# Performance work log

Hardware: AMD Instinct MI355X
Metric: run time of the kernel (lower is better)

The kernel has to match this reference:

```python
import jax, jax.numpy as jnp
import numpy as np

N_HEAD = 16
N_EMBD = 1024
TIME_EMBD = 64
EPS = 1e-5

def _ln(x, w, b):
    mu = jnp.mean(x, axis=-1, keepdims=True)
    var = jnp.mean(jnp.square(x - mu), axis=-1, keepdims=True)
    return (x - mu) * jax.lax.rsqrt(var + EPS) * w + b

def _gelu(x):
    return jax.nn.gelu(x, approximate=False)

def setup_inputs() -> dict:
    key = jax.random.key(0)
    ks = jax.random.split(key, 12)
    B, T, D, TE = 2, 2048, N_EMBD, TIME_EMBD
    C = D + TE  # 1088
    s = lambda fan_in: 1.0 / np.sqrt(fan_in)
    return {
        "z": jax.random.normal(ks[0], (B, T, D), jnp.float32),
        "t": jax.random.uniform(ks[1], (B,), jnp.float32),
        # time_mlp: Linear(1, TE) -> GELU -> Linear(TE, TE)
        "w_t1": jax.random.normal(ks[2], (1, TE), jnp.float32) * s(1),
        "b_t1": jnp.zeros((TE,), jnp.float32),
        "w_t2": jax.random.normal(ks[3], (TE, TE), jnp.float32) * s(TE),
        "b_t2": jnp.zeros((TE,), jnp.float32),
        # attention
        "ln_a_w": jnp.ones((C,), jnp.float32),
        "ln_a_b": jnp.zeros((C,), jnp.float32),
        "w_attn": jax.random.normal(ks[4], (C, 3 * D), jnp.float32) * s(C),
        "b_attn": jnp.zeros((3 * D,), jnp.float32),
        "w_proj": jax.random.normal(ks[5], (D, D), jnp.float32) * s(D),
        "b_proj": jnp.zeros((D,), jnp.float32),
        # mlp
        "ln_m_w": jnp.ones((C,), jnp.float32),
        "ln_m_b": jnp.zeros((C,), jnp.float32),
        "w_fc": jax.random.normal(ks[6], (C, 4 * D), jnp.float32) * s(C),
        "b_fc": jnp.zeros((4 * D,), jnp.float32),
        "w_fc2": jax.random.normal(ks[7], (4 * D, D), jnp.float32) * s(4 * D),
        "b_fc2": jnp.zeros((D,), jnp.float32),
    }

def reference(z, t, w_t1, b_t1, w_t2, b_t2, ln_a_w, ln_a_b, w_attn, b_attn,
              w_proj, b_proj, ln_m_w, ln_m_b, w_fc, b_fc, w_fc2, b_fc2):
    B, T, D = z.shape
    H, hd = N_HEAD, N_EMBD // N_HEAD
    # time embedding: [B, TE] broadcast over T
    t_emb = _gelu(t[:, None] @ w_t1 + b_t1) @ w_t2 + b_t2
    t_emb_bt = jnp.broadcast_to(t_emb[:, None, :], (B, T, TIME_EMBD))
    # --- attention with time-conditioned input ---
    zt = jnp.concatenate([z, t_emb_bt], axis=-1)            # [B,T,D+TE]
    x = _ln(zt, ln_a_w, ln_a_b)
    qkv = x @ w_attn + b_attn                               # [B,T,3D]
    q, k, v = jnp.split(qkv, 3, axis=-1)
    q = q.reshape(B, T, H, hd)
    k = k.reshape(B, T, H, hd)
    v = v.reshape(B, T, H, hd)
    att = jnp.einsum('bqhd,bkhd->bhqk', q, k) * (1.0 / np.sqrt(hd))
    mask = jnp.tril(jnp.ones((T, T), bool))
    att = jnp.where(mask, att, -jnp.inf)
    att = jax.nn.softmax(att, axis=-1)
    y = jnp.einsum('bhqk,bkhd->bqhd', att, v).reshape(B, T, D)
    h = y @ w_proj + b_proj                                 # [B,T,D]
    # --- mlp with time-conditioned input ---
    ht = jnp.concatenate([h, t_emb_bt], axis=-1)
    m = _ln(ht, ln_m_w, ln_m_b)
    dz = _gelu(m @ w_fc + b_fc) @ w_fc2 + b_fc2             # [B,T,D]
    return dz
```

## Files before the change

### kernel.cpp

```cpp
#include <hip/hip_runtime.h>
#include <stdint.h>
#include <math.h>

#define T_SEQ 2048
#define NHEAD 16
#define HD 64
#define DMODEL 1024
#define CDIM 1088
#define MROWS 4096

typedef uint16_t u16;
typedef __bf16 b8v __attribute__((ext_vector_type(8)));
typedef float f4v __attribute__((ext_vector_type(4)));

typedef __attribute__((address_space(3))) void lds_void;
typedef const __attribute__((address_space(1))) void glb_void;

__device__ __forceinline__ float b2f(u16 u) {
  union { uint32_t i; float f; } c; c.i = ((uint32_t)u) << 16; return c.f;
}
__device__ __forceinline__ u16 f2b(float f) {
  union { float f; uint32_t i; } c; c.f = f;
  uint32_t x = c.i;
  return (u16)((x + 0x7fffu + ((x >> 16) & 1u)) >> 16);
}
__device__ __forceinline__ float gelu_f(float x) {
  return 0.5f * x * (1.0f + erff(x * 0.70710678118654752f));
}

__global__ void time_mlp_kernel(const float* __restrict__ t, const float* __restrict__ w1,
                                const float* __restrict__ b1, const float* __restrict__ w2,
                                const float* __restrict__ b2, float* __restrict__ temb) {
  __shared__ float h1[2][64];
  int tid = threadIdx.x;
  int b = tid >> 6, i = tid & 63;
  float tv = t[b];
  h1[b][i] = gelu_f(tv * w1[i] + b1[i]);
  __syncthreads();
  float acc = b2[i];
  for (int k = 0; k < 64; ++k) acc += h1[b][k] * w2[k * 64 + i];
  temb[b * 64 + i] = acc;
}

__global__ __launch_bounds__(256) void transpose_kernel(const float* __restrict__ src,
                                                        u16* __restrict__ dst,
                                                        int R, int C) {
  __shared__ u16 tile[32][33];
  int tx = threadIdx.x & 31, ty = threadIdx.x >> 5;
  int c0 = blockIdx.x * 32, r0 = blockIdx.y * 32;
#pragma unroll
  for (int i = 0; i < 4; ++i) {
    int r = ty + i * 8;
    tile[r][tx] = f2b(src[(size_t)(r0 + r) * C + c0 + tx]);
  }
  __syncthreads();
#pragma unroll
  for (int i = 0; i < 4; ++i) {
    int c = ty + i * 8;
    dst[(size_t)(c0 + c) * R + r0 + tx] = tile[tx][c];
  }
}

__global__ __launch_bounds__(256) void ln_concat_kernel(const float* __restrict__ zf,
                                                        const u16* __restrict__ zb,
                                                        const float* __restrict__ temb,
                                                        const float* __restrict__ w,
                                                        const float* __restrict__ bvec,
                                                        u16* __restrict__ xout,
                                                        int in_f32) {
  __shared__ float red[4];
  int row = blockIdx.x;
  int b = row / T_SEQ;
  int tid = threadIdx.x;
  float v[5];
  float sum = 0.f;
#pragma unroll
  for (int i = 0; i < 5; ++i) {
    int c = tid + i * 256;
    float val = 0.f;
    if (c < CDIM) {
      if (c < DMODEL)
        val = in_f32 ? zf[(size_t)row * DMODEL + c] : b2f(zb[(size_t)row * DMODEL + c]);
      else
        val = temb[b * 64 + (c - DMODEL)];
    }
    v[i] = val;
    sum += val;
  }
#pragma unroll
  for (int off = 32; off; off >>= 1) sum += __shfl_xor(sum, off, 64);
  int wv = tid >> 6, ln = tid & 63;
  if (ln == 0) red[wv] = sum;
  __syncthreads();
  float mean = (red[0] + red[1] + red[2] + red[3]) * (1.0f / CDIM);
  __syncthreads();
  float sq = 0.f;
#pragma unroll
  for (int i = 0; i < 5; ++i) {
    int c = tid + i * 256;
    if (c < CDIM) { float d = v[i] - mean; sq += d * d; }
  }
#pragma unroll
  for (int off = 32; off; off >>= 1) sq += __shfl_xor(sq, off, 64);
  if (ln == 0) red[wv] = sq;
  __syncthreads();
  float inv = rsqrtf((red[0] + red[1] + red[2] + red[3]) * (1.0f / CDIM) + 1e-5f);
#pragma unroll
  for (int i = 0; i < 5; ++i) {
    int c = tid + i * 256;
    if (c < CDIM)
      xout[(size_t)row * CDIM + c] = f2b((v[i] - mean) * inv * w[c] + bvec[c]);
  }
}

__global__ __launch_bounds__(256) void gemm_bt_kernel(const u16* __restrict__ A,
                                                      const u16* __restrict__ Bt,
                                                      const float* __restrict__ bias,
                                                      void* __restrict__ Cout,
                                                      int M, int N, int K,
                                                      int do_gelu, int out_f32) {
  __shared__ u16 As[2][128 * 32];
  __shared__ u16 Bs[2][128 * 32];
  const int tid = threadIdx.x;
  const int wave = tid >> 6, lane = tid & 63;
  const int wr = wave >> 1, wc = wave & 1;
  const int m0 = blockIdx.x * 128;
  const int n0 = blockIdx.y * 128;
  const int lrow = lane & 15, quad = lane >> 4;
  const int srow = lane >> 2, sseg = lane & 3;

  const u16* gA0 = A  + (size_t)(m0 + wave * 32 + srow) * K + sseg * 8;
  const u16* gA1 = gA0 + (size_t)16 * K;
  const u16* gB0 = Bt + (size_t)(n0 + wave * 32 + srow) * K + sseg * 8;
  const u16* gB1 = gB0 + (size_t)16 * K;
  const int la0 = (wave * 32) * 32, la1 = (wave * 32 + 16) * 32;

  f4v acc[4][4] = {};

  __builtin_amdgcn_global_load_lds((glb_void*)gA0, (lds_void*)&As[0][la0], 16, 0, 0);
  __builtin_amdgcn_global_load_lds((glb_void*)gA1, (lds_void*)&As[0][la1], 16, 0, 0);
  __builtin_amdgcn_global_load_lds((glb_void*)gB0, (lds_void*)&Bs[0][la0], 16, 0, 0);
  __builtin_amdgcn_global_load_lds((glb_void*)gB1, (lds_void*)&Bs[0][la1], 16, 0, 0);

  int cur = 0;
  for (int k0 = 0; k0 < K; k0 += 32) {
    __syncthreads();
    if (k0 + 32 < K) {
      int nxt = cur ^ 1;
      __builtin_amdgcn_global_load_lds((glb_void*)(gA0 + k0 + 32), (lds_void*)&As[nxt][la0], 16, 0, 0);
      __builtin_amdgcn_global_load_lds((glb_void*)(gA1 + k0 + 32), (lds_void*)&As[nxt][la1], 16, 0, 0);
      __builtin_amdgcn_global_load_lds((glb_void*)(gB0 + k0 + 32), (lds_void*)&Bs[nxt][la0], 16, 0, 0);
      __builtin_amdgcn_global_load_lds((glb_void*)(gB1 + k0 + 32), (lds_void*)&Bs[nxt][la1], 16, 0, 0);
    }
    b8v af[4], bfr[4];
#pragma unroll
    for (int mi = 0; mi < 4; ++mi)
      af[mi] = *(const b8v*)(&As[cur][(wr * 64 + mi * 16 + lrow) * 32 + quad * 8]);
#pragma unroll
    for (int ni = 0; ni < 4; ++ni)
      bfr[ni] = *(const b8v*)(&Bs[cur][(wc * 64 + ni * 16 + lrow) * 32 + quad * 8]);
#pragma unroll
    for (int mi = 0; mi < 4; ++mi)
#pragma unroll
      for (int ni = 0; ni < 4; ++ni)
        acc[mi][ni] = __builtin_amdgcn_mfma_f32_16x16x32_bf16(af[mi], bfr[ni], acc[mi][ni], 0, 0, 0);
    cur ^= 1;
  }

#pragma unroll
  for (int mi = 0; mi < 4; ++mi) {
#pragma unroll
    for (int ni = 0; ni < 4; ++ni) {
      int gcol = n0 + wc * 64 + ni * 16 + lrow;
      float bv = bias[gcol];
#pragma unroll
      for (int r = 0; r < 4; ++r) {
        int grow = m0 + wr * 64 + mi * 16 + quad * 4 + r;
        float v = acc[mi][ni][r] + bv;
        if (do_gelu) v = gelu_f(v);
        if (out_f32)
          ((float*)Cout)[(size_t)grow * N + gcol] = v;
        else
          ((u16*)Cout)[(size_t)grow * N + gcol] = f2b(v);
      }
    }
  }
}

__global__ __launch_bounds__(256) void attn_mfma_kernel(const u16* __restrict__ qkv,
                                                        u16* __restrict__ y) {
  __shared__ u16 Ks[64 * 72];
  __shared__ u16 Vts[64 * 72];
  __shared__ u16 Ps[64 * 72];
  const int bh = blockIdx.x;
  const int b = bh >> 4, h = bh & 15;
  const int qt = 31 - blockIdx.y;
  const int tid = threadIdx.x, w = tid >> 6, lane = tid & 63;
  const int lrow = lane & 15, quad = lane >> 4;
  const int q0 = qt * 64;
  const int qg = q0 + w * 16 + lrow;

  b8v qf[2];
#pragma unroll
  for (int dc = 0; dc < 2; ++dc)
    qf[dc] = *(const b8v*)(qkv + (size_t)(b * T_SEQ + qg) * 3072 + h * 64 + dc * 32 + quad * 8);

  f4v oacc[4] = {};
  float mrun = -__builtin_inff(), lrun = 0.f;

  const int nch = qt + 1;
  for (int ct = 0; ct < nch; ++ct) {
    __syncthreads();
    {
      int r = tid >> 2, sg = tid & 3;
      const u16* src = qkv + (size_t)(b * T_SEQ + ct * 64 + r) * 3072 + h * 64 + 1024 + sg * 16;
      *(uint4*)(&Ks[r * 72 + sg * 16]) = *(const uint4*)(src);
      *(uint4*)(&Ks[r * 72 + sg * 16 + 8]) = *(const uint4*)(src + 8);
    }
    {
      int pr = tid >> 3, dsg = tid & 7;
      const u16* v0 = qkv + (size_t)(b * T_SEQ + ct * 64 + 2 * pr) * 3072 + h * 64 + 2048 + dsg * 8;
      uint4 a = *(const uint4*)(v0);
      uint4 bb = *(const uint4*)(v0 + 3072);
      uint32_t aw[4] = {a.x, a.y, a.z, a.w};
      uint32_t bw[4] = {bb.x, bb.y, bb.z, bb.w};
#pragma unroll
      for (int j = 0; j < 8; ++j) {
        int d = dsg * 8 + j;
        u16 ae = (u16)(aw[j >> 1] >> ((j & 1) * 16));
        u16 be = (u16)(bw[j >> 1] >> ((j & 1) * 16));
        int keyp = (2 * pr) ^ (((d >> 3) & 7) * 8);
        *(uint32_t*)(&Vts[d * 72 + keyp]) = (uint32_t)ae | ((uint32_t)be << 16);
      }
    }
    __syncthreads();

    f4v sacc[4] = {};
#pragma unroll
    for (int ks = 0; ks < 4; ++ks)
#pragma unroll
      for (int dc = 0; dc < 2; ++dc) {
        b8v kf = *(const b8v*)(&Ks[(ks * 16 + lrow) * 72 + dc * 32 + quad * 8]);
        sacc[ks] = __builtin_amdgcn_mfma_f32_16x16x32_bf16(kf, qf[dc], sacc[ks], 0, 0, 0);
      }

    bool diag = (ct == qt);
#pragma unroll
    for (int ks = 0; ks < 4; ++ks)
#pragma unroll
      for (int r = 0; r < 4; ++r) {
        float v = sacc[ks][r] * 0.125f;
        int key = ct * 64 + ks * 16 + quad * 4 + r;
        if (diag && key > qg) v = -__builtin_inff();
        sacc[ks][r] = v;
      }

    float rmax = sacc[0][0];
#pragma unroll
    for (int ks = 0; ks < 4; ++ks)
#pragma unroll
      for (int r = 0; r < 4; ++r) rmax = fmaxf(rmax, sacc[ks][r]);
    rmax = fmaxf(rmax, __shfl_xor(rmax, 16, 64));
    rmax = fmaxf(rmax, __shfl_xor(rmax, 32, 64));
    float mn = fmaxf(mrun, rmax);
    float al = __expf(mrun - mn);
    mrun = mn;
    float psum = 0.f;
#pragma unroll
    for (int ks = 0; ks < 4; ++ks)
#pragma unroll
      for (int r = 0; r < 4; ++r) {
        float p = __expf(sacc[ks][r] - mn);
        sacc[ks][r] = p;
        psum += p;
      }
    psum += __shfl_xor(psum, 16, 64);
    psum += __shfl_xor(psum, 32, 64);
    lrun = lrun * al + psum;
#pragma unroll
    for (int ds = 0; ds < 4; ++ds) oacc[ds] *= al;

#pragma unroll
    for (int ks = 0; ks < 4; ++ks) {
      ushort4 pw;
      pw.x = f2b(sacc[ks][0]); pw.y = f2b(sacc[ks][1]);
      pw.z = f2b(sacc[ks][2]); pw.w = f2b(sacc[ks][3]);
      *(ushort4*)(&Ps[(w * 16 + lrow) * 72 + ks * 16 + quad * 4]) = pw;
    }

    b8v pf[2];
#pragma unroll
    for (int kc = 0; kc < 2; ++kc)
      pf[kc] = *(const b8v*)(&Ps[(w * 16 + lrow) * 72 + kc * 32 + quad * 8]);
#pragma unroll
    for (int ds = 0; ds < 4; ++ds)
#pragma unroll
      for (int kc = 0; kc < 2; ++kc) {
        int d = ds * 16 + lrow;
        int off = (kc * 32 + quad * 8) ^ (((d >> 3) & 7) * 8);
        b8v vfv = *(const b8v*)(&Vts[d * 72 + off]);
        oacc[ds] = __builtin_amdgcn_mfma_f32_16x16x32_bf16(vfv, pf[kc], oacc[ds], 0, 0, 0);
      }
  }

  float rinv = 1.0f / lrun;
  u16* yrow = y + (size_t)(b * T_SEQ + qg) * DMODEL + h * 64;
#pragma unroll
  for (int ds = 0; ds < 4; ++ds) {
    ushort4 ov;
    ov.x = f2b(oacc[ds][0] * rinv);
    ov.y = f2b(oacc[ds][1] * rinv);
    ov.z = f2b(oacc[ds][2] * rinv);
    ov.w = f2b(oacc[ds][3] * rinv);
    *(ushort4*)(yrow + ds * 16 + quad * 4) = ov;
  }
}

extern "C" void kernel_launch(void* const* d_in, const int* in_sizes, int n_in,
                              void* d_out, int out_size, void* d_ws, size_t ws_size,
                              hipStream_t stream) {
  const float* z      = (const float*)d_in[0];
  const float* t      = (const float*)d_in[1];
  const float* w_t1   = (const float*)d_in[2];
  const float* b_t1   = (const float*)d_in[3];
  const float* w_t2   = (const float*)d_in[4];
  const float* b_t2   = (const float*)d_in[5];
  const float* ln_a_w = (const float*)d_in[6];
  const float* ln_a_b = (const float*)d_in[7];
  const float* w_attn = (const float*)d_in[8];
  const float* b_attn = (const float*)d_in[9];
  const float* w_proj = (const float*)d_in[10];
  const float* b_proj = (const float*)d_in[11];
  const float* ln_m_w = (const float*)d_in[12];
  const float* ln_m_b = (const float*)d_in[13];
  const float* w_fc   = (const float*)d_in[14];
  const float* b_fc   = (const float*)d_in[15];
  const float* w_fc2  = (const float*)d_in[16];
  const float* b_fc2  = (const float*)d_in[17];

  char* ws = (char*)d_ws;
  float* temb  = (float*)ws;
  u16* wT_attn = (u16*)(ws + 1024);
  u16* wT_proj = wT_attn + (size_t)3072 * 1088;
  u16* wT_fc   = wT_proj + (size_t)1024 * 1024;
  u16* wT_fc2  = wT_fc   + (size_t)4096 * 1088;
  u16* xbuf    = wT_fc2  + (size_t)1024 * 4096;
  u16* big     = xbuf    + (size_t)4096 * 1088;
  u16* ybuf    = big     + (size_t)4096 * 4096;
  u16* hbuf    = ybuf    + (size_t)4096 * 1024;

  time_mlp_kernel<<<dim3(1), dim3(128), 0, stream>>>(t, w_t1, b_t1, w_t2, b_t2, temb);

  transpose_kernel<<<dim3(3072 / 32, 1088 / 32), dim3(256), 0, stream>>>(w_attn, wT_attn, 1088, 3072);
  transpose_kernel<<<dim3(1024 / 32, 1024 / 32), dim3(256), 0, stream>>>(w_proj, wT_proj, 1024, 1024);
  transpose_kernel<<<dim3(4096 / 32, 1088 / 32), dim3(256), 0, stream>>>(w_fc, wT_fc, 1088, 4096);
  transpose_kernel<<<dim3(1024 / 32, 4096 / 32), dim3(256), 0, stream>>>(w_fc2, wT_fc2, 4096, 1024);

  ln_concat_kernel<<<dim3(MROWS), dim3(256), 0, stream>>>(z, (const u16*)nullptr, temb,
                                                          ln_a_w, ln_a_b, xbuf, 1);

  gemm_bt_kernel<<<dim3(MROWS / 128, 3072 / 128), dim3(256), 0, stream>>>(
      xbuf, wT_attn, b_attn, big, MROWS, 3072, 1088, 0, 0);

  attn_mfma_kernel<<<dim3(32, 32), dim3(256), 0, stream>>>(big, ybuf);

  gemm_bt_kernel<<<dim3(MROWS / 128, 1024 / 128), dim3(256), 0, stream>>>(
      ybuf, wT_proj, b_proj, hbuf, MROWS, 1024, 1024, 0, 0);

  ln_concat_kernel<<<dim3(MROWS), dim3(256), 0, stream>>>((const float*)nullptr, hbuf, temb,
                                                          ln_m_w, ln_m_b, xbuf, 0);

  gemm_bt_kernel<<<dim3(MROWS / 128, 4096 / 128), dim3(256), 0, stream>>>(
      xbuf, wT_fc, b_fc, big, MROWS, 4096, 1088, 1, 0);

  gemm_bt_kernel<<<dim3(MROWS / 128, 1024 / 128), dim3(256), 0, stream>>>(
      big, wT_fc2, b_fc2, d_out, MROWS, 1024, 4096, 0, 1);
}
```

Measured before the change: 426.8 us.

## Split-K the proj and fc2 GEMMs in two and reduce the partial sums

The two N=1024 GEMMs (attention projection and fc2) launched only 256 blocks, which underfills the GPU's CUs. A new split-K=2 GEMM writes fp32 partial results to two buffers, giving 512 blocks. The projection partials are summed inside the LN kernel through a new mode, and the fc2 partials are summed by a small add kernel. In exchange this adds fp32 partial-buffer write and read traffic, plus one extra launch for the final add.

```diff
diff --git a/kernel.cpp b/kernel.cpp
--- a/kernel.cpp
+++ b/kernel.cpp
@@ -61,13 +61,24 @@
   }
 }
 
+__global__ __launch_bounds__(256) void add2_kernel(const float4* __restrict__ a,
+                                                   const float4* __restrict__ b,
+                                                   float4* __restrict__ o, int n4) {
+  int i = blockIdx.x * 256 + threadIdx.x;
+  if (i < n4) {
+    float4 x = a[i], y = b[i];
+    o[i] = float4{x.x + y.x, x.y + y.y, x.z + y.z, x.w + y.w};
+  }
+}
+
 __global__ __launch_bounds__(256) void ln_concat_kernel(const float* __restrict__ zf,
+                                                        const float* __restrict__ zf2,
                                                         const u16* __restrict__ zb,
                                                         const float* __restrict__ temb,
                                                         const float* __restrict__ w,
                                                         const float* __restrict__ bvec,
                                                         u16* __restrict__ xout,
-                                                        int in_f32) {
+                                                        int mode) {
   __shared__ float red[4];
   int row = blockIdx.x;
   int b = row / T_SEQ;
@@ -79,10 +90,14 @@
     int c = tid + i * 256;
     float val = 0.f;
     if (c < CDIM) {
-      if (c < DMODEL)
-        val = in_f32 ? zf[(size_t)row * DMODEL + c] : b2f(zb[(size_t)row * DMODEL + c]);
-      else
+      if (c < DMODEL) {
+        size_t idx = (size_t)row * DMODEL + c;
+        if (mode == 0) val = b2f(zb[idx]);
+        else if (mode == 1) val = zf[idx];
+        else val = zf[idx] + zf2[idx];
+      } else {
         val = temb[b * 64 + (c - DMODEL)];
+      }
     }
     v[i] = val;
     sum += val;
@@ -182,6 +197,77 @@
           ((float*)Cout)[(size_t)grow * N + gcol] = v;
         else
           ((u16*)Cout)[(size_t)grow * N + gcol] = f2b(v);
+      }
+    }
+  }
+}
+
+__global__ __launch_bounds__(256) void gemm_splitk2_kernel(const u16* __restrict__ A,
+                                                           const u16* __restrict__ Bt,
+                                                           const float* __restrict__ bias,
+                                                           float* __restrict__ C0,
+                                                           float* __restrict__ C1,
+                                                           int M, int N, int K, int Kc) {
+  __shared__ u16 As[2][128 * 32];
+  __shared__ u16 Bs[2][128 * 32];
+  const int tid = threadIdx.x;
+  const int wave = tid >> 6, lane = tid & 63;
+  const int wr = wave >> 1, wc = wave & 1;
+  const int m0 = blockIdx.x * 128;
+  const int n0 = blockIdx.y * 128;
+  const int kz = blockIdx.z;
+  const int lrow = lane & 15, quad = lane >> 4;
+  const int srow = lane >> 2, sseg = lane & 3;
+
+  const u16* gA0 = A  + (size_t)(m0 + wave * 32 + srow) * K + kz * Kc + sseg * 8;
+  const u16* gA1 = gA0 + (size_t)16 * K;
+  const u16* gB0 = Bt + (size_t)(n0 + wave * 32 + srow) * K + kz * Kc + sseg * 8;
+  const u16* gB1 = gB0 + (size_t)16 * K;
+  const int la0 = (wave * 32) * 32, la1 = (wave * 32 + 16) * 32;
+
+  f4v acc[4][4] = {};
+
+  __builtin_amdgcn_global_load_lds((glb_void*)gA0, (lds_void*)&As[0][la0], 16, 0, 0);
+  __builtin_amdgcn_global_load_lds((glb_void*)gA1, (lds_void*)&As[0][la1], 16, 0, 0);
+  __builtin_amdgcn_global_load_lds((glb_void*)gB0, (lds_void*)&Bs[0][la0], 16, 0, 0);
+  __builtin_amdgcn_global_load_lds((glb_void*)gB1, (lds_void*)&Bs[0][la1], 16, 0, 0);
+
+  int cur = 0;
+  for (int k0 = 0; k0 < Kc; k0 += 32) {
+    __syncthreads();
+    if (k0 + 32 < Kc) {
+      int nxt = cur ^ 1;
+      __builtin_amdgcn_global_load_lds((glb_void*)(gA0 + k0 + 32), (lds_void*)&As[nxt][la0], 16, 0, 0);
+      __builtin_amdgcn_global_load_lds((glb_void*)(gA1 + k0 + 32), (lds_void*)&As[nxt][la1], 16, 0, 0);
+      __builtin_amdgcn_global_load_lds((glb_void*)(gB0 + k0 + 32), (lds_void*)&Bs[nxt][la0], 16, 0, 0);
+      __builtin_amdgcn_global_load_lds((glb_void*)(gB1 + k0 + 32), (lds_void*)&Bs[nxt][la1], 16, 0, 0);
+    }
+    b8v af[4], bfr[4];
+#pragma unroll
+    for (int mi = 0; mi < 4; ++mi)
+      af[mi] = *(const b8v*)(&As[cur][(wr * 64 + mi * 16 + lrow) * 32 + quad * 8]);
+#pragma unroll
+    for (int ni = 0; ni < 4; ++ni)
+      bfr[ni] = *(const b8v*)(&Bs[cur][(wc * 64 + ni * 16 + lrow) * 32 + quad * 8]);
+#pragma unroll
+    for (int mi = 0; mi < 4; ++mi)
+#pragma unroll
+      for (int ni = 0; ni < 4; ++ni)
+        acc[mi][ni] = __builtin_amdgcn_mfma_f32_16x16x32_bf16(af[mi], bfr[ni], acc[mi][ni], 0, 0, 0);
+    cur ^= 1;
+  }
+
+  float* C = kz ? C1 : C0;
+#pragma unroll
+  for (int mi = 0; mi < 4; ++mi) {
+#pragma unroll
+    for (int ni = 0; ni < 4; ++ni) {
+      int gcol = n0 + wc * 64 + ni * 16 + lrow;
+      float bv = (kz == 0) ? bias[gcol] : 0.f;
+#pragma unroll
+      for (int r = 0; r < 4; ++r) {
+        int grow = m0 + wr * 64 + mi * 16 + quad * 4 + r;
+        C[(size_t)grow * N + gcol] = acc[mi][ni][r] + bv;
       }
     }
   }
@@ -347,7 +433,8 @@
   u16* xbuf    = wT_fc2  + (size_t)1024 * 4096;
   u16* big     = xbuf    + (size_t)4096 * 1088;
   u16* ybuf    = big     + (size_t)4096 * 4096;
-  u16* hbuf    = ybuf    + (size_t)4096 * 1024;
+  float* p0    = (float*)(ybuf + (size_t)4096 * 1024);
+  float* p1    = p0 + (size_t)4096 * 1024;
 
   time_mlp_kernel<<<dim3(1), dim3(128), 0, stream>>>(t, w_t1, b_t1, w_t2, b_t2, temb);
 
@@ -356,23 +443,26 @@
   transpose_kernel<<<dim3(4096 / 32, 1088 / 32), dim3(256), 0, stream>>>(w_fc, wT_fc, 1088, 4096);
   transpose_kernel<<<dim3(1024 / 32, 4096 / 32), dim3(256), 0, stream>>>(w_fc2, wT_fc2, 4096, 1024);
 
-  ln_concat_kernel<<<dim3(MROWS), dim3(256), 0, stream>>>(z, (const u16*)nullptr, temb,
-                                                          ln_a_w, ln_a_b, xbuf, 1);
+  ln_concat_kernel<<<dim3(MROWS), dim3(256), 0, stream>>>(
+      z, (const float*)nullptr, (const u16*)nullptr, temb, ln_a_w, ln_a_b, xbuf, 1);
 
   gemm_bt_kernel<<<dim3(MROWS / 128, 3072 / 128), dim3(256), 0, stream>>>(
       xbuf, wT_attn, b_attn, big, MROWS, 3072, 1088, 0, 0);
 
   attn_mfma_kernel<<<dim3(32, 32), dim3(256), 0, stream>>>(big, ybuf);
 
-  gemm_bt_kernel<<<dim3(MROWS / 128, 1024 / 128), dim3(256), 0, stream>>>(
-      ybuf, wT_proj, b_proj, hbuf, MROWS, 1024, 1024, 0, 0);
-
-  ln_concat_kernel<<<dim3(MROWS), dim3(256), 0, stream>>>((const float*)nullptr, hbuf, temb,
-                                                          ln_m_w, ln_m_b, xbuf, 0);
+  gemm_splitk2_kernel<<<dim3(MROWS / 128, 1024 / 128, 2), dim3(256), 0, stream>>>(
+      ybuf, wT_proj, b_proj, p0, p1, MROWS, 1024, 1024, 512);
+
+  ln_concat_kernel<<<dim3(MROWS), dim3(256), 0, stream>>>(
+      p0, p1, (const u16*)nullptr, temb, ln_m_w, ln_m_b, xbuf, 2);
 
   gemm_bt_kernel<<<dim3(MROWS / 128, 4096 / 128), dim3(256), 0, stream>>>(
       xbuf, wT_fc, b_fc, big, MROWS, 4096, 1088, 1, 0);
 
-  gemm_bt_kernel<<<dim3(MROWS / 128, 1024 / 128), dim3(256), 0, stream>>>(
-      big, wT_fc2, b_fc2, d_out, MROWS, 1024, 4096, 0, 1);
-}
+  gemm_splitk2_kernel<<<dim3(MROWS / 128, 1024 / 128, 2), dim3(256), 0, stream>>>(
+      big, wT_fc2, b_fc2, p0, p1, MROWS, 1024, 4096, 2048);
+
+  add2_kernel<<<dim3((MROWS * 1024 / 4 + 255) / 256), dim3(256), 0, stream>>>(
+      (const float4*)p0, (const float4*)p1, (float4*)d_out, MROWS * 1024 / 4);
+}
```

New measurement: 407.0 us. 1.05x faster.
